# Kernel optimization log

Hardware: AMD Instinct MI355X
Metric: run time of the kernel (lower is better)

## Reference

```python
import jax, jax.numpy as jnp
import numpy as np
import math

IN_CH = 512
OUT_CH = 512
K = 3
STYLE_DIM = 512
EPS = 1e-8


def setup_inputs() -> dict:
    key = jax.random.key(0)
    k1, k2, k3, k4 = jax.random.split(key, 4)
    x = jax.random.normal(k1, (16, IN_CH, 64, 64), dtype=jnp.float32)
    style = jax.random.normal(k2, (16, STYLE_DIM), dtype=jnp.float32)
    weight = jax.random.normal(k3, (OUT_CH, IN_CH, K, K), dtype=jnp.float32)
    affine_w = jax.random.normal(k4, (IN_CH, STYLE_DIM), dtype=jnp.float32)
    affine_b = jnp.ones((IN_CH,), dtype=jnp.float32)  # bias_init=1.0
    return {"x": x, "style": style, "weight": weight,
            "affine_w": affine_w, "affine_b": affine_b}


def reference(x, style, weight, affine_w, affine_b):
    # EqualizedLinear: weight_scale = 1/sqrt(style_dim), lr_multiplier = 1
    w_scale = 1.0 / math.sqrt(STYLE_DIM)
    s = style @ (affine_w * w_scale).T + affine_b  # [B, Ci]

    # Demodulation factor: sigma_inv[b,o] = rsqrt(sum_{i,k,k} (w[o,i,k,k]*s[b,i])^2 + eps)
    wsq = jnp.sum(weight ** 2, axis=(2, 3))               # [Co, Ci]
    sigma_inv = jax.lax.rsqrt(jnp.einsum('oi,bi->bo', wsq, s ** 2) + EPS)  # [B, Co]

    # Modulated grouped conv == scale input per-channel, shared-weight conv,
    # scale output per-channel (conv is linear in the weight).
    x_mod = x * s[:, :, None, None]                        # [B, Ci, H, W]
    pad = K // 2
    y = jax.lax.conv_general_dilated(
        x_mod, weight,
        window_strides=(1, 1),
        padding=((pad, pad), (pad, pad)),
        dimension_numbers=('NCHW', 'OIHW', 'NCHW'))       # [B, Co, H, W]
    y = y * sigma_inv[:, :, None, None]
    return y
```

## Files before the change

kernel.cpp:

```cpp
#include <hip/hip_runtime.h>
#include <hip/hip_bf16.h>

#define BATCH 16
#define CI    512
#define CO    512
#define IMG   64
#define HP    66
#define NPIX  4096
#define NTAP  9

typedef __bf16  bf16x8  __attribute__((ext_vector_type(8)));
typedef float   floatx4 __attribute__((ext_vector_type(4)));

#define OFF_S     0u
#define OFF_SIG   32768u
#define OFF_WSQ   65536u
#define OFF_WBF   1114112u
#define OFF_XPAD  5832704u
#define XPAD_BYTES 71368704u
#define WS_NEEDED (OFF_XPAD + XPAD_BYTES)

__global__ void k_style(const float* __restrict__ style, const float* __restrict__ aw,
                        const float* __restrict__ ab, float* __restrict__ s_out)
{
    __shared__ float st[512];
    int b = blockIdx.x;
    int t = threadIdx.x;
    st[t]       = style[b * 512 + t];
    st[t + 256] = style[b * 512 + t + 256];
    __syncthreads();
    int i = blockIdx.y * 256 + t;
    const float4* awr = (const float4*)(aw + (size_t)i * 512);
    float sum = 0.f;
#pragma unroll 8
    for (int k = 0; k < 128; ++k) {
        float4 v = awr[k];
        sum += v.x * st[4 * k] + v.y * st[4 * k + 1] + v.z * st[4 * k + 2] + v.w * st[4 * k + 3];
    }
    s_out[b * 512 + i] = sum * 0.04419417382415922f + ab[i];
}

__global__ void k_wprep(const float* __restrict__ wgt, float* __restrict__ wsq,
                        unsigned short* __restrict__ wbf)
{
    int idx = blockIdx.x * 256 + threadIdx.x;
    const float* p = wgt + (size_t)idx * 9;
    float q = 0.f;
#pragma unroll
    for (int t9 = 0; t9 < 9; ++t9) {
        float v = p[t9];
        q += v * v;
        __hip_bfloat16 hv = __float2bfloat16(v);
        wbf[t9 * 262144 + idx] = *(unsigned short*)&hv;
    }
    wsq[idx] = q;
}

__global__ void k_sigma(const float* __restrict__ s_in, const float* __restrict__ wsq,
                        float* __restrict__ sig)
{
    __shared__ float s2[512];
    int b = blockIdx.x, t = threadIdx.x;
    float a0 = s_in[b * 512 + t], a1 = s_in[b * 512 + t + 256];
    s2[t] = a0 * a0;
    s2[t + 256] = a1 * a1;
    __syncthreads();
    int o = blockIdx.y * 256 + t;
    const float4* wr = (const float4*)(wsq + (size_t)o * 512);
    float sum = 0.f;
#pragma unroll 8
    for (int k = 0; k < 128; ++k) {
        float4 v = wr[k];
        sum += v.x * s2[4 * k] + v.y * s2[4 * k + 1] + v.z * s2[4 * k + 2] + v.w * s2[4 * k + 3];
    }
    sig[b * 512 + o] = rsqrtf(sum + 1e-8f);
}

__global__ void k_xmod(const float* __restrict__ x, const float* __restrict__ s_in,
                       unsigned short* __restrict__ xpad)
{
    __shared__ unsigned short tile[64 * 128];
    __shared__ float sm_s[128];
    int b = blockIdx.x, h = blockIdx.y, quarter = blockIdx.z;
    int ci0 = quarter << 7;
    int t = threadIdx.x;
    if (t < 128) sm_s[t] = s_in[b * 512 + ci0 + t];
    __syncthreads();

    int w0 = (t & 15) << 2;
    int cp = (t >> 4) << 1;
#pragma unroll
    for (int i = 0; i < 4; ++i) {
        int cl = (i << 5) + cp;
        float sv0 = sm_s[cl], sv1 = sm_s[cl + 1];
        float4 v0 = *(const float4*)(x + (((size_t)(b * 512 + ci0 + cl)) << 12) + (h << 6) + w0);
        float4 v1 = *(const float4*)(x + (((size_t)(b * 512 + ci0 + cl + 1)) << 12) + (h << 6) + w0);
        float a0[4] = {v0.x, v0.y, v0.z, v0.w};
        float a1[4] = {v1.x, v1.y, v1.z, v1.w};
#pragma unroll
        for (int j = 0; j < 4; ++j) {
            int wq = w0 + j;
            __hip_bfloat16 h0 = __float2bfloat16(a0[j] * sv0);
            __hip_bfloat16 h1 = __float2bfloat16(a1[j] * sv1);
            unsigned int packed = (unsigned int)(*(unsigned short*)&h0)
                                | ((unsigned int)(*(unsigned short*)&h1) << 16);
            int off = (wq << 7) + ((((cl >> 3) ^ ((wq >> 2) & 7))) << 3) + (cl & 7);
            *(unsigned int*)&tile[off] = packed;
        }
    }
    __syncthreads();

    int q = t & 15;
    size_t rowb = (size_t)((b * 66 + h + 1) * 66 + 1) * 512 + ci0;
#pragma unroll
    for (int i = 0; i < 4; ++i) {
        int wq = (i << 4) + (t >> 4);
        int off = (wq << 7) + ((q ^ ((wq >> 2) & 7)) << 3);
        uint4 v = *(const uint4*)&tile[off];
        *(uint4*)(xpad + rowb + (size_t)wq * 512 + (q << 3)) = v;
    }

    uint4 z = {0u, 0u, 0u, 0u};
    if (t < 32) {
        int wp = (t >> 4) * 65;
        *(uint4*)(xpad + (size_t)((b * 66 + h + 1) * 66 + wp) * 512 + ci0 + ((t & 15) << 3)) = z;
    }
    if (h == 0 || h == 63) {
        int hp = (h == 0) ? 0 : 65;
        size_t base = (size_t)(b * 66 + hp) * 66 * 512 + ci0;
        for (int idx = t; idx < 66 * 16; idx += 256) {
            int p = idx >> 4, c = idx & 15;
            *(uint4*)(xpad + base + (size_t)p * 512 + (c << 3)) = z;
        }
    }
}

__device__ __forceinline__ void gload16(const void* g, void* l)
{
    __builtin_amdgcn_global_load_lds(
        (const __attribute__((address_space(1))) unsigned int*)g,
        (__attribute__((address_space(3))) unsigned int*)l, 16, 0, 0);
}

__global__ __launch_bounds__(256, 2)
void k_conv(const unsigned short* __restrict__ xpad, const unsigned short* __restrict__ wbf,
            const float* __restrict__ sig, float* __restrict__ y)
{
    __shared__ unsigned short A_lds[2 * 3 * 4096];
    __shared__ unsigned short B_lds[2 * 4224];
    int t = threadIdx.x;
    int w = t >> 6, l = t & 63;
    int wr = w >> 1, wc = w & 1;
    int bx = blockIdx.x;
    int b = bx >> 7, rem = bx & 127;
    int co_t = rem >> 5, pix_t = rem & 31;
    int o_base = co_t << 7;
    int h0 = pix_t << 1;

    const char* wb = (const char*)wbf;
    const char* xb = (const char*)xpad;

    int idx0 = (w << 6) + l;
    int idx1 = idx0 + 256;
    int asw = (((idx0 & 3) ^ ((idx0 >> 3) & 3)) << 4);
    int aof0 = ((o_base + (idx0 >> 2)) << 10) + asw;
    int aof1 = aof0 + 65536;

    int r0 = idx0 >> 2;
    int bof0 = ((b * 66 + h0) * 66 + r0) * 1024 + (((idx0 & 3) ^ ((r0 >> 1) & 3)) << 4);
    int r1 = idx1 >> 2;
    int sr1 = (r1 >= 66) ? 1 : 0;
    int wp1 = r1 - 66 * sr1;
    int bof1 = ((b * 66 + h0 + sr1) * 66 + wp1) * 1024 + (((idx1 & 3) ^ ((r1 >> 1) & 3)) << 4);
    int idxt = 512 + (w << 2) + l;
    int rt = 128 + w;
    int boft = ((b * 66 + h0 + 1) * 66 + 62 + w) * 1024 + (((idxt & 3) ^ ((rt >> 1) & 3)) << 4);

    int lr = l & 15, q = l >> 4;
    int fa = wr * 2048 + lr * 32 + ((q ^ ((lr >> 1) & 3)) << 3);
    int fbo[3][4];
#pragma unroll
    for (int kw = 0; kw < 3; ++kw)
#pragma unroll
        for (int j = 0; j < 4; ++j) {
            int sp = wc * 66 + j * 16 + lr + kw;
            fbo[kw][j] = sp * 32 + ((q ^ ((sp >> 1) & 3)) << 3);
        }

    floatx4 acc[4][4];
#pragma unroll
    for (int i = 0; i < 4; ++i)
#pragma unroll
        for (int j = 0; j < 4; ++j)
            acc[i][j] = (floatx4){0.f, 0.f, 0.f, 0.f};

    auto stage = [&](int step, int nb) {
        int kh = step >> 4;
        int cic = step & 15;
        const char* wk = wb + kh * 1572864 + (cic << 6);
        const char* xk = xb + kh * 67584 + (cic << 6);
        char* ab = (char*)(A_lds + nb * 12288) + (w << 10);
        char* bbase = (char*)(B_lds + nb * 4224);
        gload16(wk + aof0,           ab);
        gload16(wk + aof1,           ab + 4096);
        gload16(wk + 524288 + aof0,  ab + 8192);
        gload16(wk + 524288 + aof1,  ab + 12288);
        gload16(wk + 1048576 + aof0, ab + 16384);
        gload16(wk + 1048576 + aof1, ab + 20480);
        gload16(xk + bof0, bbase + (w << 10));
        gload16(xk + bof1, bbase + 4096 + (w << 10));
        if (l < 4) gload16(xk + boft, bbase + ((512 + (w << 2)) << 4));
    };

    stage(0, 0);
    asm volatile("s_waitcnt vmcnt(0)" ::: "memory");
    __builtin_amdgcn_s_barrier();
    __builtin_amdgcn_sched_barrier(0);

    int cur = 0;
    for (int step = 0; step < 48; ++step) {
        if (step < 47) stage(step + 1, cur ^ 1);

        const unsigned short* Ab = A_lds + cur * 12288;
        const unsigned short* Bb = B_lds + cur * 4224;
#pragma unroll
        for (int kw = 0; kw < 3; ++kw) {
            bf16x8 bfr[4], af[4];
#pragma unroll
            for (int j = 0; j < 4; ++j) bfr[j] = *(const bf16x8*)&Bb[fbo[kw][j]];
#pragma unroll
            for (int i = 0; i < 4; ++i) af[i]  = *(const bf16x8*)&Ab[kw * 4096 + fa + i * 512];
            __builtin_amdgcn_s_setprio(1);
#pragma unroll
            for (int i = 0; i < 4; ++i)
#pragma unroll
                for (int j = 0; j < 4; ++j)
                    acc[i][j] = __builtin_amdgcn_mfma_f32_16x16x32_bf16(af[i], bfr[j], acc[i][j], 0, 0, 0);
            __builtin_amdgcn_s_setprio(0);
        }

        asm volatile("s_waitcnt vmcnt(0)" ::: "memory");
        __builtin_amdgcn_s_barrier();
        __builtin_amdgcn_sched_barrier(0);
        cur ^= 1;
    }

    int col = l & 15, quad = l >> 4;
    const float* sb = sig + b * 512;
#pragma unroll
    for (int i = 0; i < 4; ++i) {
        int ob = o_base + wr * 64 + i * 16 + quad * 4;
#pragma unroll
        for (int r = 0; r < 4; ++r) {
            int o = ob + r;
            float sv = sb[o];
            float* yrow = y + (((size_t)(b * 512 + o)) << 12);
#pragma unroll
            for (int j = 0; j < 4; ++j) {
                int pix = (pix_t << 7) + wc * 64 + j * 16 + col;
                yrow[pix] = acc[i][j][r] * sv;
            }
        }
    }
}

extern "C" void kernel_launch(void* const* d_in, const int* in_sizes, int n_in,
                              void* d_out, int out_size, void* d_ws, size_t ws_size,
                              hipStream_t stream)
{
    const float* x        = (const float*)d_in[0];
    const float* style    = (const float*)d_in[1];
    const float* weight   = (const float*)d_in[2];
    const float* affine_w = (const float*)d_in[3];
    const float* affine_b = (const float*)d_in[4];
    float* y = (float*)d_out;

    if (ws_size < (size_t)WS_NEEDED) return;

    char* ws = (char*)d_ws;
    float*          s_buf = (float*)(ws + OFF_S);
    float*          sig   = (float*)(ws + OFF_SIG);
    float*          wsq   = (float*)(ws + OFF_WSQ);
    unsigned short* wbf   = (unsigned short*)(ws + OFF_WBF);
    unsigned short* xpad  = (unsigned short*)(ws + OFF_XPAD);

    k_style<<<dim3(16, 2), 256, 0, stream>>>(style, affine_w, affine_b, s_buf);
    k_wprep<<<1024, 256, 0, stream>>>(weight, wsq, wbf);
    k_xmod<<<dim3(16, 64, 4), 256, 0, stream>>>(x, s_buf, xpad);
    k_sigma<<<dim3(16, 2), 256, 0, stream>>>(s_buf, wsq, sig);
    k_conv<<<2048, 256, 0, stream>>>(xpad, wbf, sig, y);
}
```

Baseline: 567.1 us.

## Software-pipeline LDS fragment loads against MFMAs and overlap barrier with last tap

```diff
diff --git a/kernel.cpp b/kernel.cpp
--- a/kernel.cpp
+++ b/kernel.cpp
@@ -43,8 +43,17 @@
 __global__ void k_wprep(const float* __restrict__ wgt, float* __restrict__ wsq,
                         unsigned short* __restrict__ wbf)
 {
-    int idx = blockIdx.x * 256 + threadIdx.x;
-    const float* p = wgt + (size_t)idx * 9;
+    __shared__ float sw[2304];
+    int t = threadIdx.x;
+    int blk = blockIdx.x;
+    const float4* src = (const float4*)(wgt + (size_t)blk * 2304);
+#pragma unroll
+    for (int k = 0; k < 2; ++k) ((float4*)sw)[t + 256 * k] = src[t + 256 * k];
+    if (t < 64) ((float4*)sw)[t + 512] = src[t + 512];
+    __syncthreads();
+
+    int idx = blk * 256 + t;
+    const float* p = sw + t * 9;
     float q = 0.f;
 #pragma unroll
     for (int t9 = 0; t9 < 9; ++t9) {
@@ -223,25 +232,40 @@
 
         const unsigned short* Ab = A_lds + cur * 12288;
         const unsigned short* Bb = B_lds + cur * 4224;
-#pragma unroll
-        for (int kw = 0; kw < 3; ++kw) {
-            bf16x8 bfr[4], af[4];
-#pragma unroll
-            for (int j = 0; j < 4; ++j) bfr[j] = *(const bf16x8*)&Bb[fbo[kw][j]];
-#pragma unroll
-            for (int i = 0; i < 4; ++i) af[i]  = *(const bf16x8*)&Ab[kw * 4096 + fa + i * 512];
-            __builtin_amdgcn_s_setprio(1);
-#pragma unroll
-            for (int i = 0; i < 4; ++i)
-#pragma unroll
-                for (int j = 0; j < 4; ++j)
-                    acc[i][j] = __builtin_amdgcn_mfma_f32_16x16x32_bf16(af[i], bfr[j], acc[i][j], 0, 0, 0);
-            __builtin_amdgcn_s_setprio(0);
-        }
-
-        asm volatile("s_waitcnt vmcnt(0)" ::: "memory");
+
+        bf16x8 af0[4], bf0[4], af1[4], bf1[4], af2[4], bf2[4];
+#pragma unroll
+        for (int j = 0; j < 4; ++j) bf0[j] = *(const bf16x8*)&Bb[fbo[0][j]];
+#pragma unroll
+        for (int i = 0; i < 4; ++i) af0[i] = *(const bf16x8*)&Ab[fa + i * 512];
+#pragma unroll
+        for (int j = 0; j < 4; ++j) bf1[j] = *(const bf16x8*)&Bb[fbo[1][j]];
+#pragma unroll
+        for (int i = 0; i < 4; ++i) af1[i] = *(const bf16x8*)&Ab[4096 + fa + i * 512];
+#pragma unroll
+        for (int i = 0; i < 4; ++i)
+#pragma unroll
+            for (int j = 0; j < 4; ++j)
+                acc[i][j] = __builtin_amdgcn_mfma_f32_16x16x32_bf16(af0[i], bf0[j], acc[i][j], 0, 0, 0);
+#pragma unroll
+        for (int j = 0; j < 4; ++j) bf2[j] = *(const bf16x8*)&Bb[fbo[2][j]];
+#pragma unroll
+        for (int i = 0; i < 4; ++i) af2[i] = *(const bf16x8*)&Ab[8192 + fa + i * 512];
+#pragma unroll
+        for (int i = 0; i < 4; ++i)
+#pragma unroll
+            for (int j = 0; j < 4; ++j)
+                acc[i][j] = __builtin_amdgcn_mfma_f32_16x16x32_bf16(af1[i], bf1[j], acc[i][j], 0, 0, 0);
+
+        asm volatile("s_waitcnt vmcnt(0) lgkmcnt(0)" ::: "memory");
         __builtin_amdgcn_s_barrier();
-        __builtin_amdgcn_sched_barrier(0);
+
+#pragma unroll
+        for (int i = 0; i < 4; ++i)
+#pragma unroll
+            for (int j = 0; j < 4; ++j)
+                acc[i][j] = __builtin_amdgcn_mfma_f32_16x16x32_bf16(af2[i], bf2[j], acc[i][j], 0, 0, 0);
+
         cur ^= 1;
     }
 
```

New measurement: 599.5 us. 5.7% more time.

## Load conv weight fragments directly into registers instead of staging through LDS

Applied to the files above, without the earlier changes.

```diff
diff --git a/kernel.cpp b/kernel.cpp
--- a/kernel.cpp
+++ b/kernel.cpp
@@ -43,8 +43,17 @@
 __global__ void k_wprep(const float* __restrict__ wgt, float* __restrict__ wsq,
                         unsigned short* __restrict__ wbf)
 {
-    int idx = blockIdx.x * 256 + threadIdx.x;
-    const float* p = wgt + (size_t)idx * 9;
+    __shared__ float sw[2304];
+    int t = threadIdx.x;
+    int blk = blockIdx.x;
+    const float4* src = (const float4*)(wgt + (size_t)blk * 2304);
+#pragma unroll
+    for (int k = 0; k < 2; ++k) ((float4*)sw)[t + 256 * k] = src[t + 256 * k];
+    if (t < 64) ((float4*)sw)[t + 512] = src[t + 512];
+    __syncthreads();
+
+    int idx = blk * 256 + t;
+    const float* p = sw + t * 9;
     float q = 0.f;
 #pragma unroll
     for (int t9 = 0; t9 < 9; ++t9) {
@@ -146,7 +155,6 @@
 void k_conv(const unsigned short* __restrict__ xpad, const unsigned short* __restrict__ wbf,
             const float* __restrict__ sig, float* __restrict__ y)
 {
-    __shared__ unsigned short A_lds[2 * 3 * 4096];
     __shared__ unsigned short B_lds[2 * 4224];
     int t = threadIdx.x;
     int w = t >> 6, l = t & 63;
@@ -162,10 +170,6 @@
 
     int idx0 = (w << 6) + l;
     int idx1 = idx0 + 256;
-    int asw = (((idx0 & 3) ^ ((idx0 >> 3) & 3)) << 4);
-    int aof0 = ((o_base + (idx0 >> 2)) << 10) + asw;
-    int aof1 = aof0 + 65536;
-
     int r0 = idx0 >> 2;
     int bof0 = ((b * 66 + h0) * 66 + r0) * 1024 + (((idx0 & 3) ^ ((r0 >> 1) & 3)) << 4);
     int r1 = idx1 >> 2;
@@ -177,7 +181,7 @@
     int boft = ((b * 66 + h0 + 1) * 66 + 62 + w) * 1024 + (((idxt & 3) ^ ((rt >> 1) & 3)) << 4);
 
     int lr = l & 15, q = l >> 4;
-    int fa = wr * 2048 + lr * 32 + ((q ^ ((lr >> 1) & 3)) << 3);
+    const char* pA = wb + (((size_t)(o_base + wr * 64 + lr)) << 10) + (q << 4);
     int fbo[3][4];
 #pragma unroll
     for (int kw = 0; kw < 3; ++kw)
@@ -194,55 +198,65 @@
         for (int j = 0; j < 4; ++j)
             acc[i][j] = (floatx4){0.f, 0.f, 0.f, 0.f};
 
-    auto stage = [&](int step, int nb) {
+    bf16x8 A0[12], A1[12];
+
+    auto stageB = [&](int step, int nb) {
         int kh = step >> 4;
         int cic = step & 15;
-        const char* wk = wb + kh * 1572864 + (cic << 6);
         const char* xk = xb + kh * 67584 + (cic << 6);
-        char* ab = (char*)(A_lds + nb * 12288) + (w << 10);
         char* bbase = (char*)(B_lds + nb * 4224);
-        gload16(wk + aof0,           ab);
-        gload16(wk + aof1,           ab + 4096);
-        gload16(wk + 524288 + aof0,  ab + 8192);
-        gload16(wk + 524288 + aof1,  ab + 12288);
-        gload16(wk + 1048576 + aof0, ab + 16384);
-        gload16(wk + 1048576 + aof1, ab + 20480);
         gload16(xk + bof0, bbase + (w << 10));
         gload16(xk + bof1, bbase + 4096 + (w << 10));
         if (l < 4) gload16(xk + boft, bbase + ((512 + (w << 2)) << 4));
     };
 
-    stage(0, 0);
+    auto loadA = [&](int step, bf16x8 (&Ad)[12]) {
+        int kh = step >> 4;
+        int cic = step & 15;
+        const char* base = pA + kh * 1572864 + (cic << 6);
+#pragma unroll
+        for (int kw = 0; kw < 3; ++kw)
+#pragma unroll
+            for (int i = 0; i < 4; ++i)
+                Ad[kw * 4 + i] = *(const bf16x8*)(base + kw * 524288 + i * 16384);
+    };
+
+    auto compute = [&](const unsigned short* Bb, const bf16x8 (&A)[12]) {
+#pragma unroll
+        for (int kw = 0; kw < 3; ++kw) {
+            bf16x8 bfr[4];
+#pragma unroll
+            for (int j = 0; j < 4; ++j) bfr[j] = *(const bf16x8*)&Bb[fbo[kw][j]];
+#pragma unroll
+            for (int i = 0; i < 4; ++i)
+#pragma unroll
+                for (int j = 0; j < 4; ++j)
+                    acc[i][j] = __builtin_amdgcn_mfma_f32_16x16x32_bf16(A[kw * 4 + i], bfr[j], acc[i][j], 0, 0, 0);
+        }
+    };
+
+    stageB(0, 0);
+    loadA(0, A0);
     asm volatile("s_waitcnt vmcnt(0)" ::: "memory");
     __builtin_amdgcn_s_barrier();
     __builtin_amdgcn_sched_barrier(0);
 
-    int cur = 0;
-    for (int step = 0; step < 48; ++step) {
-        if (step < 47) stage(step + 1, cur ^ 1);
-
-        const unsigned short* Ab = A_lds + cur * 12288;
-        const unsigned short* Bb = B_lds + cur * 4224;
-#pragma unroll
-        for (int kw = 0; kw < 3; ++kw) {
-            bf16x8 bfr[4], af[4];
-#pragma unroll
-            for (int j = 0; j < 4; ++j) bfr[j] = *(const bf16x8*)&Bb[fbo[kw][j]];
-#pragma unroll
-            for (int i = 0; i < 4; ++i) af[i]  = *(const bf16x8*)&Ab[kw * 4096 + fa + i * 512];
-            __builtin_amdgcn_s_setprio(1);
-#pragma unroll
-            for (int i = 0; i < 4; ++i)
-#pragma unroll
-                for (int j = 0; j < 4; ++j)
-                    acc[i][j] = __builtin_amdgcn_mfma_f32_16x16x32_bf16(af[i], bfr[j], acc[i][j], 0, 0, 0);
-            __builtin_amdgcn_s_setprio(0);
-        }
-
-        asm volatile("s_waitcnt vmcnt(0)" ::: "memory");
+    for (int s2 = 0; s2 < 24; ++s2) {
+        int e = s2 * 2;
+        stageB(e + 1, 1);
+        loadA(e + 1, A1);
+        compute(B_lds, A0);
+        asm volatile("s_waitcnt vmcnt(0) lgkmcnt(0)" ::: "memory");
         __builtin_amdgcn_s_barrier();
         __builtin_amdgcn_sched_barrier(0);
-        cur ^= 1;
+        if (e + 2 < 48) {
+            stageB(e + 2, 0);
+            loadA(e + 2, A0);
+        }
+        compute(B_lds + 4224, A1);
+        asm volatile("s_waitcnt vmcnt(0) lgkmcnt(0)" ::: "memory");
+        __builtin_amdgcn_s_barrier();
+        __builtin_amdgcn_sched_barrier(0);
     }
 
     int col = l & 15, quad = l >> 4;
```

New measurement: 888.1 us. +56.6%, slower.
